# Kernel optimization log

Hardware: AMD Instinct MI355X
Metric: run time of the kernel (lower is better)

## Reference

```python
import jax, jax.numpy as jnp
import numpy as np

C = 768; NH = 12; HD = C // NH; P = 16; IMG = 256; HS = IMG // P  # 16x16 patch grid
WIN = 7; HWP = WIN // 2  # half window (pad)
DEPTH = 12; MLP = 4 * C
B = 32; T = 1
OFFS = [(dh, dw) for dh in range(WIN) for dw in range(WIN)]


def ln(x, g, b, eps=1e-5):
    mu = jnp.mean(x, axis=-1, keepdims=True)
    var = jnp.mean((x - mu) ** 2, axis=-1, keepdims=True)
    return (x - mu) * jax.lax.rsqrt(var + eps) * g + b


def local_attn(x, qkv_w, proj_w, proj_b):
    # x: (B, N, C) with N = HS*HS (T=1); sliding-window attention, zero-padded keys
    Bc, N, _ = x.shape
    qkv = (x @ qkv_w.T).reshape(Bc, N, 3, NH, HD)
    q, k, v = [jnp.transpose(qkv[:, :, i], (0, 2, 1, 3)).reshape(Bc, NH, HS, HS, HD)
               for i in range(3)]
    scale = HD ** -0.5
    kp = jnp.pad(k, ((0, 0), (0, 0), (HWP, HWP), (HWP, HWP), (0, 0)))
    vp = jnp.pad(v, ((0, 0), (0, 0), (HWP, HWP), (HWP, HWP), (0, 0)))
    # per-offset logits; padded (zero) keys give logit 0, matching torch's zero-pad softmax
    scores = jnp.stack([
        jnp.einsum('bnhwd,bnhwd->bnhw', q, kp[:, :, dh:dh + HS, dw:dw + HS]) * scale
        for dh, dw in OFFS], axis=-1)  # (B, NH, HS, HS, 49)
    attn = jax.nn.softmax(scores, axis=-1)
    out = sum(attn[..., i, None] * vp[:, :, dh:dh + HS, dw:dw + HS]
              for i, (dh, dw) in enumerate(OFFS))  # (B, NH, HS, HS, HD)
    out = jnp.transpose(out, (0, 2, 3, 1, 4)).reshape(Bc, N, C)
    return out @ proj_w.T + proj_b


def global_attn(x, in_w, in_b, out_w, out_b):
    Bc, N, _ = x.shape
    qkv = x @ in_w.T + in_b
    q, k, v = jnp.split(qkv, 3, axis=-1)
    hds = lambda t: t.reshape(Bc, N, NH, HD).transpose(0, 2, 1, 3)
    q, k, v = hds(q), hds(k), hds(v)
    s = jnp.einsum('bnqd,bnkd->bnqk', q, k) * (HD ** -0.5)
    a = jax.nn.softmax(s, axis=-1)
    o = jnp.einsum('bnqk,bnkd->bnqd', a, v).transpose(0, 2, 1, 3).reshape(Bc, N, C)
    return o @ out_w.T + out_b


def setup_inputs() -> dict:
    key = jax.random.key(0)
    ks = iter(jax.random.split(key, 40))
    s = 0.02
    inp = {
        'x': jax.random.normal(next(ks), (B, T, 3, IMG, IMG), jnp.float32),
        'aspect_ratio': jax.random.uniform(next(ks), (B,), jnp.float32),
        'conv_w': jax.random.normal(next(ks), (C, 3, P, P), jnp.float32) * s,
        'conv_b': jnp.zeros((C,), jnp.float32),
        'pe_g': jnp.ones((C,), jnp.float32), 'pe_b': jnp.zeros((C,), jnp.float32),
        'ar_token': jax.random.normal(next(ks), (1, 1, C), jnp.float32) * s,
        'pos_embed': jax.random.normal(next(ks), (1, 100 * HS * HS + 1, C), jnp.float32) * s,
        'ln1_g': jnp.ones((DEPTH, C), jnp.float32), 'ln1_b': jnp.zeros((DEPTH, C), jnp.float32),
        'ln2_g': jnp.ones((DEPTH, C), jnp.float32), 'ln2_b': jnp.zeros((DEPTH, C), jnp.float32),
        'loc_qkv_w': jax.random.normal(next(ks), (6, 3 * C, C), jnp.float32) * s,
        'loc_proj_w': jax.random.normal(next(ks), (6, C, C), jnp.float32) * s,
        'loc_proj_b': jnp.zeros((6, C), jnp.float32),
        'glob_in_w': jax.random.normal(next(ks), (6, 3 * C, C), jnp.float32) * s,
        'glob_in_b': jnp.zeros((6, 3 * C), jnp.float32),
        'glob_out_w': jax.random.normal(next(ks), (6, C, C), jnp.float32) * s,
        'glob_out_b': jnp.zeros((6, C), jnp.float32),
        'mlp_w1': jax.random.normal(next(ks), (DEPTH, MLP, C), jnp.float32) * s,
        'mlp_b1': jnp.zeros((DEPTH, MLP), jnp.float32),
        'mlp_w2': jax.random.normal(next(ks), (DEPTH, C, MLP), jnp.float32) * s,
        'mlp_b2': jnp.zeros((DEPTH, C), jnp.float32),
        'fin_g': jnp.ones((C,), jnp.float32), 'fin_b': jnp.zeros((C,), jnp.float32),
    }
    return inp


def reference(x, aspect_ratio, conv_w, conv_b, pe_g, pe_b, ar_token, pos_embed,
              ln1_g, ln1_b, ln2_g, ln2_b,
              loc_qkv_w, loc_proj_w, loc_proj_b,
              glob_in_w, glob_in_b, glob_out_w, glob_out_b,
              mlp_w1, mlp_b1, mlp_w2, mlp_b2, fin_g, fin_b):
    Bc, Tc, Ci, Hi, Wi = x.shape
    # patch embed: non-overlapping conv == block reshape + einsum
    xf = x.reshape(Bc * Tc, Ci, HS, P, HS, P)
    patches = jnp.einsum('bchpwq,ecpq->bhwe', xf, conv_w) + conv_b
    patches = patches.reshape(Bc, Tc * HS * HS, C)
    patches = ln(patches, pe_g, pe_b)
    # aspect ratio token
    ar = ar_token * (1.0 + aspect_ratio[:, None, None] * 0.1)  # (B,1,C)
    h = jnp.concatenate([patches, ar], axis=1)
    h = h + pos_embed[:, :h.shape[1], :]
    for i in range(DEPTH):
        if i % 2 == 0:  # local attention block (AR token stripped, N == HS*HS+1)
            li = i // 2
            tok, art = h[:, :-1], h[:, -1:]
            tok = tok + local_attn(ln(tok, ln1_g[i], ln1_b[i]),
                                   loc_qkv_w[li], loc_proj_w[li], loc_proj_b[li])
            h = jnp.concatenate([tok, art], axis=1)
        else:
            gi = i // 2
            h = h + global_attn(ln(h, ln1_g[i], ln1_b[i]),
                                glob_in_w[gi], glob_in_b[gi], glob_out_w[gi], glob_out_b[gi])
        m = ln(h, ln2_g[i], ln2_b[i])
        m = jax.nn.gelu(m @ mlp_w1[i].T + mlp_b1[i], approximate=False)
        h = h + m @ mlp_w2[i].T + mlp_b2[i]
    return ln(h, fin_g, fin_b)
```

## Files before the change

### kernel.cpp

```cpp
#include <hip/hip_runtime.h>
#include <cmath>

#define NHEADS 12
#define NTOK   257
#define BATCH  32
#define ROWS   (BATCH*NTOK)
#define PROWS  (BATCH*256)
#define GTPAD  288

typedef __attribute__((ext_vector_type(8))) short short8;
typedef __attribute__((ext_vector_type(8))) unsigned short u16x8;
typedef __attribute__((ext_vector_type(4))) float f32x4;

__device__ __forceinline__ unsigned short f2bf(float f) {
    unsigned u = __float_as_uint(f);
    unsigned r = (u + 0x7FFFu + ((u >> 16) & 1u)) >> 16;
    return (unsigned short)r;
}
__device__ __forceinline__ float b2f(unsigned short us) {
    return __uint_as_float((unsigned)us << 16);
}
__device__ __forceinline__ void gload16(const void* g, void* l) {
    __builtin_amdgcn_global_load_lds(
        (const __attribute__((address_space(1))) void*)g,
        (__attribute__((address_space(3))) void*)l, 16, 0, 0);
}

template<bool BIAS, bool GELU, bool RES, bool SKIPAR, bool OUTBF>
__global__ __launch_bounds__(256) void gemm_bf16(
    const unsigned short* __restrict__ A, const unsigned short* __restrict__ W,
    const float* __restrict__ bias, void* __restrict__ outv,
    int M, int N, int K)
{
    __shared__ unsigned short As[2][128 * 64];
    __shared__ unsigned short Bs[2][128 * 64];
    const int tid = threadIdx.x;
    const int lane = tid & 63, wid = tid >> 6;
    const int wr = wid >> 1, wc = wid & 1;

    const int gx = gridDim.x;
    const int nwg = gx * gridDim.y;
    const int orig = blockIdx.y * gx + blockIdx.x;
    const int q8 = nwg >> 3, r8 = nwg & 7;
    const int xcd = orig & 7, lid = orig >> 3;
    const int wg = (xcd < r8 ? xcd * (q8 + 1) : r8 * (q8 + 1) + (xcd - r8) * q8) + lid;
    const int bn = (wg % gx) * 128;
    const int bm = (wg / gx) * 128;

    f32x4 acc[4][4];
    #pragma unroll
    for (int i = 0; i < 4; i++)
        #pragma unroll
        for (int j = 0; j < 4; j++) acc[i][j] = (f32x4)0.f;

    const int l15 = lane & 15;
    const int lg  = lane >> 4;
    const int sw  = l15 & 7;

    auto stage = [&](int buf, int k0) {
        #pragma unroll
        for (int it = 0; it < 4; it++) {
            int f = it * 256 + tid;
            int row = f >> 3;
            int g = (f & 7) ^ (row & 7);
            gload16(A + (size_t)(bm + row) * K + k0 + g * 8, &As[buf][f * 8]);
            gload16(W + (size_t)(bn + row) * K + k0 + g * 8, &Bs[buf][f * 8]);
        }
    };

    const int nt = K >> 6;
    stage(0, 0);
    __syncthreads();

    int buf = 0;
    for (int t = 0; t < nt; t++) {
        if (t + 1 < nt) stage(buf ^ 1, (t + 1) << 6);
        #pragma unroll
        for (int kk = 0; kk < 2; kk++) {
            short8 af[4], bf[4];
            #pragma unroll
            for (int i = 0; i < 4; i++) {
                int row = wr * 64 + i * 16 + l15;
                af[i] = *(const short8*)&As[buf][row * 64 + (((kk * 4 + lg) ^ sw)) * 8];
            }
            #pragma unroll
            for (int j = 0; j < 4; j++) {
                int row = wc * 64 + j * 16 + l15;
                bf[j] = *(const short8*)&Bs[buf][row * 64 + (((kk * 4 + lg) ^ sw)) * 8];
            }
            #pragma unroll
            for (int i = 0; i < 4; i++)
                #pragma unroll
                for (int j = 0; j < 4; j++)
                    acc[i][j] = __builtin_amdgcn_mfma_f32_16x16x32_bf16(af[i], bf[j], acc[i][j], 0, 0, 0);
        }
        __syncthreads();
        buf ^= 1;
    }

    float bcol[4];
    #pragma unroll
    for (int j = 0; j < 4; j++)
        bcol[j] = BIAS ? bias[bn + wc * 64 + j * 16 + l15] : 0.f;

    #pragma unroll
    for (int i = 0; i < 4; i++) {
        #pragma unroll
        for (int r = 0; r < 4; r++) {
            int row = bm + wr * 64 + i * 16 + lg * 4 + r;
            if (row >= M) continue;
            if (SKIPAR && (row % NTOK) == (NTOK - 1)) continue;
            #pragma unroll
            for (int j = 0; j < 4; j++) {
                int col = bn + wc * 64 + j * 16 + l15;
                float v = acc[i][j][r] + bcol[j];
                if (GELU) v = 0.5f * v * (1.0f + erff(v * 0.70710678118654752f));
                size_t idx = (size_t)row * N + col;
                if (OUTBF) {
                    ((unsigned short*)outv)[idx] = f2bf(v);
                } else {
                    float* o = (float*)outv;
                    if (RES) o[idx] += v; else o[idx] = v;
                }
            }
        }
    }
}

template<bool OUTBF>
__global__ __launch_bounds__(256) void ln_kernel(
    const float* __restrict__ in, void* __restrict__ outv,
    const float* __restrict__ g, const float* __restrict__ bparm, int rows)
{
    int gw = blockIdx.x * 4 + (threadIdx.x >> 6);
    int lane = threadIdx.x & 63;
    if (gw >= rows) return;
    const float* x = in + (size_t)gw * 768;
    float4 v[3];
    #pragma unroll
    for (int i = 0; i < 3; i++) v[i] = *(const float4*)(x + i * 256 + lane * 4);
    float s = 0.f;
    #pragma unroll
    for (int i = 0; i < 3; i++) s += v[i].x + v[i].y + v[i].z + v[i].w;
    #pragma unroll
    for (int off = 32; off >= 1; off >>= 1) s += __shfl_xor(s, off, 64);
    float mu = s * (1.f / 768.f);
    float q = 0.f;
    #pragma unroll
    for (int i = 0; i < 3; i++) {
        float dx = v[i].x - mu, dy = v[i].y - mu, dz = v[i].z - mu, dw = v[i].w - mu;
        q += dx * dx + dy * dy + dz * dz + dw * dw;
    }
    #pragma unroll
    for (int off = 32; off >= 1; off >>= 1) q += __shfl_xor(q, off, 64);
    float rstd = rsqrtf(q * (1.f / 768.f) + 1e-5f);
    #pragma unroll
    for (int i = 0; i < 3; i++) {
        float4 gg = *(const float4*)(g + i * 256 + lane * 4);
        float4 bb = *(const float4*)(bparm + i * 256 + lane * 4);
        float rx = (v[i].x - mu) * rstd * gg.x + bb.x;
        float ry = (v[i].y - mu) * rstd * gg.y + bb.y;
        float rz = (v[i].z - mu) * rstd * gg.z + bb.z;
        float rw = (v[i].w - mu) * rstd * gg.w + bb.w;
        if (OUTBF) {
            ushort4 u;
            u.x = f2bf(rx); u.y = f2bf(ry); u.z = f2bf(rz); u.w = f2bf(rw);
            *(ushort4*)((unsigned short*)outv + (size_t)gw * 768 + i * 256 + lane * 4) = u;
        } else {
            *(float4*)((float*)outv + (size_t)gw * 768 + i * 256 + lane * 4) =
                make_float4(rx, ry, rz, rw);
        }
    }
}

__global__ __launch_bounds__(256) void f2b_kernel(
    const float* __restrict__ in, unsigned short* __restrict__ out, int n4)
{
    int i = blockIdx.x * 256 + threadIdx.x;
    if (i >= n4) return;
    float4 v = ((const float4*)in)[i];
    ushort4 u;
    u.x = f2bf(v.x); u.y = f2bf(v.y); u.z = f2bf(v.z); u.w = f2bf(v.w);
    ((ushort4*)out)[i] = u;
}

__global__ __launch_bounds__(256) void gather_patches(
    const float* __restrict__ x, unsigned short* __restrict__ A)
{
    int row = blockIdx.x;
    int b = row >> 8;
    int pp = row & 255;
    int ph = pp >> 4, pw = pp & 15;
    const float* xb = x + (size_t)b * 196608;
    for (int e = threadIdx.x; e < 768; e += 256) {
        int c = e >> 8;
        int r = e & 255;
        int p = r >> 4, q = r & 15;
        A[(size_t)row * 768 + e] = f2bf(xb[(size_t)c * 65536 + (ph * 16 + p) * 256 + pw * 16 + q]);
    }
}

__global__ __launch_bounds__(256) void build_h_kernel(
    const unsigned short* __restrict__ lnp, const float* __restrict__ pos,
    const float* __restrict__ artok, const float* __restrict__ aspect,
    float* __restrict__ h)
{
    int row = blockIdx.x;
    int b = row / NTOK;
    int t = row - b * NTOK;
    float* hp = h + (size_t)row * 768;
    int e = threadIdx.x;
    if (t < 256) {
        const unsigned short* lp = lnp + ((size_t)b * 256 + t) * 768;
        const float* pp = pos + (size_t)t * 768;
        #pragma unroll
        for (int i = 0; i < 3; i++) { int c = e + i * 256; hp[c] = b2f(lp[c]) + pp[c]; }
    } else {
        float f = 1.0f + aspect[b] * 0.1f;
        const float* pp = pos + (size_t)256 * 768;
        #pragma unroll
        for (int i = 0; i < 3; i++) { int c = e + i * 256; hp[c] = artok[c] * f + pp[c]; }
    }
}

__global__ __launch_bounds__(256) void transpose_v(
    const unsigned short* __restrict__ qkv, unsigned short* __restrict__ vt)
{
    __shared__ unsigned short T[64][72];
    const int bh = blockIdx.x;
    const int b = bh / NHEADS, nh = bh % NHEADS;
    const unsigned short* vbase = qkv + (size_t)b * NTOK * 2304 + 1536 + nh * 64;
    unsigned short* obase = vt + (size_t)bh * 64 * GTPAD;
    const int tid = threadIdx.x;

    for (int t0 = 0; t0 < GTPAD; t0 += 64) {
        #pragma unroll
        for (int rnd = 0; rnd < 2; rnd++) {
            int tl = rnd * 32 + (tid >> 3);
            int d0 = (tid & 7) * 8;
            int tok = t0 + tl;
            u16x8 v;
            if (tok < NTOK) {
                v = *(const u16x8*)(vbase + (size_t)tok * 2304 + d0);
            } else {
                #pragma unroll
                for (int i = 0; i < 8; i++) v[i] = 0;
            }
            #pragma unroll
            for (int i = 0; i < 8; i++) T[d0 + i][tl] = v[i];
        }
        __syncthreads();
        int d = tid >> 2, ts = (tid & 3) * 16;
        if (t0 + ts < GTPAD) {
            u16x8 o0, o1;
            #pragma unroll
            for (int i = 0; i < 8; i++) { o0[i] = T[d][ts + i]; o1[i] = T[d][ts + 8 + i]; }
            *(u16x8*)(obase + (size_t)d * GTPAD + t0 + ts) = o0;
            *(u16x8*)(obase + (size_t)d * GTPAD + t0 + ts + 8) = o1;
        }
        __syncthreads();
    }
}

__global__ __launch_bounds__(256) void local_attn_mfma(
    const unsigned short* __restrict__ qkv, const unsigned short* __restrict__ vt,
    unsigned short* __restrict__ out)
{
    __shared__ unsigned short P[4][16 * 136];
    const int wid = threadIdx.x >> 6, lane = threadIdx.x & 63;
    const int gw = blockIdx.x * 4 + wid;
    const int bh = gw >> 4, h0 = gw & 15;
    const int b = bh / NHEADS, nh = bh % NHEADS;
    const int l15 = lane & 15, lg = lane >> 4;
    const unsigned short* base = qkv + (size_t)b * NTOK * 2304 + nh * 64;
    const unsigned short* vtb = vt + (size_t)bh * 64 * GTPAD;
    unsigned short* Pw = P[wid];

    const int qtok = h0 * 16 + l15;
    short8 qf0 = *(const short8*)(base + (size_t)qtok * 2304 + lg * 8);
    short8 qf1 = *(const short8*)(base + (size_t)qtok * 2304 + 32 + lg * 8);

    int r0 = h0 - 3; r0 = r0 < 0 ? 0 : (r0 > 8 ? 8 : r0);

    f32x4 s[8];
    #pragma unroll
    for (int i = 0; i < 8; i++) {
        const unsigned short* kr = base + (size_t)((r0 + i) * 16 + l15) * 2304 + 768;
        short8 kf0 = *(const short8*)(kr + lg * 8);
        short8 kf1 = *(const short8*)(kr + 32 + lg * 8);
        f32x4 z = (f32x4)0.f;
        z = __builtin_amdgcn_mfma_f32_16x16x32_bf16(kf0, qf0, z, 0, 0, 0);
        z = __builtin_amdgcn_mfma_f32_16x16x32_bf16(kf1, qf1, z, 0, 0, 0);
        s[i] = z;
    }

    const int vlo = l15 - 3 < 0 ? 0 : l15 - 3;
    const int vhi = l15 + 3 > 15 ? 15 : l15 + 3;
    const int rlo = h0 - 3 < 0 ? 0 : h0 - 3;
    const int rhi = h0 + 3 > 15 ? 15 : h0 + 3;
    const int n_oob = 49 - (rhi - rlo + 1) * (vhi - vlo + 1);
    float m = n_oob > 0 ? 0.f : -1e30f;
    float sv[32];
    #pragma unroll
    for (int i = 0; i < 8; i++) {
        int kh = r0 + i;
        bool rowok = (kh >= rlo) && (kh <= rhi);
        #pragma unroll
        for (int r = 0; r < 4; r++) {
            int kw = lg * 4 + r;
            bool ok = rowok && (kw >= vlo) && (kw <= vhi);
            float xx = ok ? s[i][r] * 0.125f : -1e30f;
            sv[i * 4 + r] = xx;
            m = fmaxf(m, xx);
        }
    }
    m = fmaxf(m, __shfl_xor(m, 16, 64));
    m = fmaxf(m, __shfl_xor(m, 32, 64));
    float tsum = 0.f;
    #pragma unroll
    for (int i = 0; i < 8; i++) {
        float p0 = __expf(sv[i * 4 + 0] - m);
        float p1 = __expf(sv[i * 4 + 1] - m);
        float p2 = __expf(sv[i * 4 + 2] - m);
        float p3 = __expf(sv[i * 4 + 3] - m);
        tsum += p0 + p1 + p2 + p3;
        unsigned u0 = (unsigned)f2bf(p0) | ((unsigned)f2bf(p1) << 16);
        unsigned u1 = (unsigned)f2bf(p2) | ((unsigned)f2bf(p3) << 16);
        *(uint2*)((char*)Pw + l15 * 272 + i * 32 + lg * 8) = make_uint2(u0, u1);
    }
    tsum += __shfl_xor(tsum, 16, 64);
    tsum += __shfl_xor(tsum, 32, 64);
    float denom = tsum + (float)n_oob * __expf(-m);
    __syncthreads();

    f32x4 acc[4];
    #pragma unroll
    for (int d = 0; d < 4; d++) acc[d] = (f32x4)0.f;
    #pragma unroll
    for (int kt = 0; kt < 128; kt += 32) {
        short8 pf = *(const short8*)((char*)Pw + l15 * 272 + kt * 2 + lg * 16);
        #pragma unroll
        for (int d = 0; d < 4; d++) {
            short8 vf = *(const short8*)(vtb + (size_t)(d * 16 + l15) * GTPAD + r0 * 16 + kt + lg * 8);
            acc[d] = __builtin_amdgcn_mfma_f32_16x16x32_bf16(vf, pf, acc[d], 0, 0, 0);
        }
    }

    float inv = 1.f / denom;
    unsigned short* op = out + ((size_t)b * NTOK + qtok) * 768 + nh * 64;
    #pragma unroll
    for (int d = 0; d < 4; d++) {
        ushort4 o;
        o.x = f2bf(acc[d][0] * inv);
        o.y = f2bf(acc[d][1] * inv);
        o.z = f2bf(acc[d][2] * inv);
        o.w = f2bf(acc[d][3] * inv);
        *(ushort4*)(op + d * 16 + lg * 4) = o;
    }
}

__global__ __launch_bounds__(64) void global_attn_mfma(
    const unsigned short* __restrict__ qkv, const unsigned short* __restrict__ vt,
    unsigned short* __restrict__ out)
{
    __shared__ uint4 Pbuf[80];
    unsigned short* P = (unsigned short*)Pbuf;
    const int blk = blockIdx.x;
    const int bh = blk / 17, qt = blk % 17;
    const int b = bh / NHEADS, nh = bh % NHEADS;
    const int lane = threadIdx.x;
    const int l15 = lane & 15, lg = lane >> 4;
    const unsigned short* base = qkv + (size_t)b * NTOK * 2304 + nh * 64;
    const unsigned short* vtb = vt + (size_t)bh * 64 * GTPAD;

    int qrow = qt * 16 + l15;
    const bool qvalid = qrow < NTOK;
    if (!qvalid) qrow = NTOK - 1;
    short8 qf[2];
    qf[0] = *(const short8*)(base + (size_t)qrow * 2304 + lg * 8);
    qf[1] = *(const short8*)(base + (size_t)qrow * 2304 + 32 + lg * 8);

    f32x4 acc[4];
    #pragma unroll
    for (int i = 0; i < 4; i++) acc[i] = (f32x4)0.f;
    float m = -1e30f, l = 0.f;

    for (int kt = 0; kt < GTPAD; kt += 32) {
        f32x4 s[2];
        #pragma unroll
        for (int hh = 0; hh < 2; hh++) {
            int krow = kt + hh * 16 + l15;
            if (krow > NTOK - 1) krow = NTOK - 1;
            short8 kf0 = *(const short8*)(base + (size_t)krow * 2304 + 768 + lg * 8);
            short8 kf1 = *(const short8*)(base + (size_t)krow * 2304 + 768 + 32 + lg * 8);
            f32x4 z = (f32x4)0.f;
            z = __builtin_amdgcn_mfma_f32_16x16x32_bf16(kf0, qf[0], z, 0, 0, 0);
            z = __builtin_amdgcn_mfma_f32_16x16x32_bf16(kf1, qf[1], z, 0, 0, 0);
            s[hh] = z;
        }
        float sv[8];
        float mt = -1e30f;
        #pragma unroll
        for (int hh = 0; hh < 2; hh++)
            #pragma unroll
            for (int r = 0; r < 4; r++) {
                int key = kt + hh * 16 + lg * 4 + r;
                float v = s[hh][r] * 0.125f;
                if (key >= NTOK) v = -1e30f;
                sv[hh * 4 + r] = v;
                mt = fmaxf(mt, v);
            }
        mt = fmaxf(mt, __shfl_xor(mt, 16, 64));
        mt = fmaxf(mt, __shfl_xor(mt, 32, 64));
        float mn = fmaxf(m, mt);
        float cf = __expf(m - mn);
        float tsum = 0.f;
        unsigned short pb[8];
        #pragma unroll
        for (int i = 0; i < 8; i++) {
            float p = __expf(sv[i] - mn);
            tsum += p;
            pb[i] = f2bf(p);
        }
        tsum += __shfl_xor(tsum, 16, 64);
        tsum += __shfl_xor(tsum, 32, 64);
        l = l * cf + tsum;
        m = mn;
        #pragma unroll
        for (int i = 0; i < 4; i++) acc[i] *= cf;

        unsigned u0 = (unsigned)pb[0] | ((unsigned)pb[1] << 16);
        unsigned u1 = (unsigned)pb[2] | ((unsigned)pb[3] << 16);
        unsigned u2 = (unsigned)pb[4] | ((unsigned)pb[5] << 16);
        unsigned u3 = (unsigned)pb[6] | ((unsigned)pb[7] << 16);
        *(uint2*)((char*)P + l15 * 80 + lg * 8)      = make_uint2(u0, u1);
        *(uint2*)((char*)P + l15 * 80 + 32 + lg * 8) = make_uint2(u2, u3);
        __syncthreads();
        short8 pf = *(const short8*)((char*)P + l15 * 80 + lg * 16);
        #pragma unroll
        for (int d = 0; d < 4; d++) {
            short8 vf = *(const short8*)(vtb + (size_t)(d * 16 + l15) * GTPAD + kt + lg * 8);
            acc[d] = __builtin_amdgcn_mfma_f32_16x16x32_bf16(vf, pf, acc[d], 0, 0, 0);
        }
        __syncthreads();
    }

    if (qvalid) {
        float inv = 1.f / l;
        unsigned short* op = out + ((size_t)b * NTOK + qrow) * 768 + nh * 64;
        #pragma unroll
        for (int d = 0; d < 4; d++) {
            ushort4 o;
            o.x = f2bf(acc[d][0] * inv);
            o.y = f2bf(acc[d][1] * inv);
            o.z = f2bf(acc[d][2] * inv);
            o.w = f2bf(acc[d][3] * inv);
            *(ushort4*)(op + d * 16 + lg * 4) = o;
        }
    }
}

extern "C" void kernel_launch(void* const* d_in, const int* in_sizes, int n_in,
                              void* d_out, int out_size, void* d_ws, size_t ws_size,
                              hipStream_t stream)
{
    const float* x       = (const float*)d_in[0];
    const float* aspect  = (const float*)d_in[1];
    const float* conv_w  = (const float*)d_in[2];
    const float* conv_b  = (const float*)d_in[3];
    const float* pe_g    = (const float*)d_in[4];
    const float* pe_b    = (const float*)d_in[5];
    const float* ar_tok  = (const float*)d_in[6];
    const float* pos     = (const float*)d_in[7];
    const float* ln1_g   = (const float*)d_in[8];
    const float* ln1_b   = (const float*)d_in[9];
    const float* ln2_g   = (const float*)d_in[10];
    const float* ln2_b   = (const float*)d_in[11];
    const float* loc_qkv_w  = (const float*)d_in[12];
    const float* loc_proj_w = (const float*)d_in[13];
    const float* loc_proj_b = (const float*)d_in[14];
    const float* glob_in_w  = (const float*)d_in[15];
    const float* glob_in_b  = (const float*)d_in[16];
    const float* glob_out_w = (const float*)d_in[17];
    const float* glob_out_b = (const float*)d_in[18];
    const float* mlp_w1  = (const float*)d_in[19];
    const float* mlp_b1  = (const float*)d_in[20];
    const float* mlp_w2  = (const float*)d_in[21];
    const float* mlp_b2  = (const float*)d_in[22];
    const float* fin_g   = (const float*)d_in[23];
    const float* fin_b   = (const float*)d_in[24];

    char* w = (char*)d_ws;
    float*          h     = (float*)w;
    unsigned short* lnb   = (unsigned short*)(w + 25264128);
    unsigned short* qkvb  = (unsigned short*)(w + 37896192);
    unsigned short* attnb = (unsigned short*)(w + 75792384);
    unsigned short* mlpb  = (unsigned short*)(w + 88424448);
    float*          pembf = (float*)mlpb;
    unsigned short* vtb   = mlpb;
    char* wp = w + 138952704;
    unsigned short* wconv  = (unsigned short*)wp;               wp += 1179648;
    unsigned short* wlqkv  = (unsigned short*)wp;               wp += 21233664;
    unsigned short* wlproj = (unsigned short*)wp;               wp += 7077888;
    unsigned short* wgin   = (unsigned short*)wp;               wp += 21233664;
    unsigned short* wgout  = (unsigned short*)wp;               wp += 7077888;
    unsigned short* wm1    = (unsigned short*)wp;               wp += 56623104;
    unsigned short* wm2    = (unsigned short*)wp;               wp += 56623104;

    auto cvt = [&](const float* src, unsigned short* dst, int n) {
        int n4 = n / 4;
        f2b_kernel<<<(n4 + 255) / 256, 256, 0, stream>>>(src, dst, n4);
    };
    cvt(conv_w,     wconv,  768 * 768);
    cvt(loc_qkv_w,  wlqkv,  6 * 2304 * 768);
    cvt(loc_proj_w, wlproj, 6 * 768 * 768);
    cvt(glob_in_w,  wgin,   6 * 2304 * 768);
    cvt(glob_out_w, wgout,  6 * 768 * 768);
    cvt(mlp_w1,     wm1,    12 * 3072 * 768);
    cvt(mlp_w2,     wm2,    12 * 768 * 3072);

    gather_patches<<<PROWS, 256, 0, stream>>>(x, qkvb);
    gemm_bf16<true, false, false, false, false><<<dim3(6, 64), 256, 0, stream>>>(
        qkvb, wconv, conv_b, pembf, PROWS, 768, 768);
    ln_kernel<true><<<PROWS / 4, 256, 0, stream>>>(pembf, attnb, pe_g, pe_b, PROWS);
    build_h_kernel<<<ROWS, 256, 0, stream>>>(attnb, pos, ar_tok, aspect, h);

    const int mt = (ROWS + 127) / 128;
    for (int i = 0; i < 12; i++) {
        int half = i / 2;
        ln_kernel<true><<<(ROWS + 3) / 4, 256, 0, stream>>>(h, lnb, ln1_g + i * 768, ln1_b + i * 768, ROWS);
        if ((i & 1) == 0) {
            gemm_bf16<false, false, false, false, true><<<dim3(18, mt), 256, 0, stream>>>(
                lnb, wlqkv + (size_t)half * 2304 * 768, nullptr, qkvb, ROWS, 2304, 768);
            transpose_v<<<BATCH * NHEADS, 256, 0, stream>>>(qkvb, vtb);
            local_attn_mfma<<<BATCH * NHEADS * 16 / 4, 256, 0, stream>>>(qkvb, vtb, attnb);
            gemm_bf16<true, false, true, true, false><<<dim3(6, mt), 256, 0, stream>>>(
                attnb, wlproj + (size_t)half * 768 * 768, loc_proj_b + half * 768, h, ROWS, 768, 768);
        } else {
            gemm_bf16<true, false, false, false, true><<<dim3(18, mt), 256, 0, stream>>>(
                lnb, wgin + (size_t)half * 2304 * 768, glob_in_b + half * 2304, qkvb, ROWS, 2304, 768);
            transpose_v<<<BATCH * NHEADS, 256, 0, stream>>>(qkvb, vtb);
            global_attn_mfma<<<BATCH * NHEADS * 17, 64, 0, stream>>>(qkvb, vtb, attnb);
            gemm_bf16<true, false, true, false, false><<<dim3(6, mt), 256, 0, stream>>>(
                attnb, wgout + (size_t)half * 768 * 768, glob_out_b + half * 768, h, ROWS, 768, 768);
        }
        ln_kernel<true><<<(ROWS + 3) / 4, 256, 0, stream>>>(h, lnb, ln2_g + i * 768, ln2_b + i * 768, ROWS);
        gemm_bf16<true, true, false, false, true><<<dim3(24, mt), 256, 0, stream>>>(
            lnb, wm1 + (size_t)i * 3072 * 768, mlp_b1 + i * 3072, mlpb, ROWS, 3072, 768);
        gemm_bf16<true, false, true, false, false><<<dim3(6, mt), 256, 0, stream>>>(
            mlpb, wm2 + (size_t)i * 768 * 3072, mlp_b2 + i * 768, h, ROWS, 768, 3072);
    }
    ln_kernel<false><<<(ROWS + 3) / 4, 256, 0, stream>>>(h, (float*)d_out, fin_g, fin_b, ROWS);
}
```

Measured before the change: 3.682 ms.

## Fuse V transpose into QKV GEMM epilogue and use tanh GELU

The QKV GEMM epilogue now writes the V columns straight into the transposed per-head vt buffer, so the separate transpose_v kernel is no longer launched. A small kernel zeroes the padded tail of vt once per layer, and vt gets its own workspace region. Separately, the exact erf GELU is replaced by a tanh approximation built on __expf, which lowers epilogue cost but changes numerics relative to the exact-GELU reference. The transposed V stores are strided scatters, so they may write memory less efficiently than the old tiled transpose.

```diff
diff --git a/kernel.cpp b/kernel.cpp
--- a/kernel.cpp
+++ b/kernel.cpp
@@ -25,11 +25,18 @@
         (const __attribute__((address_space(1))) void*)g,
         (__attribute__((address_space(3))) void*)l, 16, 0, 0);
 }
-
-template<bool BIAS, bool GELU, bool RES, bool SKIPAR, bool OUTBF>
+__device__ __forceinline__ float gelu_f(float x) {
+    float y = 0.7978845608f * (x + 0.044715f * x * x * x);
+    float e = __expf(2.f * y);
+    float t = 1.f - 2.f / (e + 1.f);
+    return 0.5f * x * (1.f + t);
+}
+
+template<bool BIAS, bool GELU, bool RES, bool SKIPAR, bool OUTBF, bool VT>
 __global__ __launch_bounds__(256) void gemm_bf16(
     const unsigned short* __restrict__ A, const unsigned short* __restrict__ W,
     const float* __restrict__ bias, void* __restrict__ outv,
+    unsigned short* __restrict__ vt,
     int M, int N, int K)
 {
     __shared__ unsigned short As[2][128 * 64];
@@ -62,9 +69,9 @@
         for (int it = 0; it < 4; it++) {
             int f = it * 256 + tid;
             int row = f >> 3;
-            int g = (f & 7) ^ (row & 7);
-            gload16(A + (size_t)(bm + row) * K + k0 + g * 8, &As[buf][f * 8]);
-            gload16(W + (size_t)(bn + row) * K + k0 + g * 8, &Bs[buf][f * 8]);
+            int gc = (f & 7) ^ (row & 7);
+            gload16(A + (size_t)(bm + row) * K + k0 + gc * 8, &As[buf][f * 8]);
+            gload16(W + (size_t)(bn + row) * K + k0 + gc * 8, &Bs[buf][f * 8]);
         }
     };
 
@@ -110,14 +117,22 @@
             int row = bm + wr * 64 + i * 16 + lg * 4 + r;
             if (row >= M) continue;
             if (SKIPAR && (row % NTOK) == (NTOK - 1)) continue;
+            int bb = 0, tok = 0;
+            if (VT) { bb = row / NTOK; tok = row - bb * NTOK; }
             #pragma unroll
             for (int j = 0; j < 4; j++) {
                 int col = bn + wc * 64 + j * 16 + l15;
                 float v = acc[i][j][r] + bcol[j];
-                if (GELU) v = 0.5f * v * (1.0f + erff(v * 0.70710678118654752f));
+                if (GELU) v = gelu_f(v);
                 size_t idx = (size_t)row * N + col;
                 if (OUTBF) {
-                    ((unsigned short*)outv)[idx] = f2bf(v);
+                    if (VT && col >= 1536) {
+                        int c = col - 1536;
+                        int nh = c >> 6, d = c & 63;
+                        vt[(size_t)((bb * NHEADS + nh) * 64 + d) * GTPAD + tok] = f2bf(v);
+                    } else {
+                        ((unsigned short*)outv)[idx] = f2bf(v);
+                    }
                 } else {
                     float* o = (float*)outv;
                     if (RES) o[idx] += v; else o[idx] = v;
@@ -125,6 +140,13 @@
             }
         }
     }
+}
+
+__global__ __launch_bounds__(256) void zero_vt_pad(unsigned short* __restrict__ vt)
+{
+    int t = blockIdx.x * 256 + threadIdx.x;
+    int bhd = t >> 2, ch = t & 3;
+    *(uint4*)(vt + (size_t)bhd * GTPAD + 256 + ch * 8) = make_uint4(0u, 0u, 0u, 0u);
 }
 
 template<bool OUTBF>
@@ -220,45 +242,6 @@
         const float* pp = pos + (size_t)256 * 768;
         #pragma unroll
         for (int i = 0; i < 3; i++) { int c = e + i * 256; hp[c] = artok[c] * f + pp[c]; }
-    }
-}
-
-__global__ __launch_bounds__(256) void transpose_v(
-    const unsigned short* __restrict__ qkv, unsigned short* __restrict__ vt)
-{
-    __shared__ unsigned short T[64][72];
-    const int bh = blockIdx.x;
-    const int b = bh / NHEADS, nh = bh % NHEADS;
-    const unsigned short* vbase = qkv + (size_t)b * NTOK * 2304 + 1536 + nh * 64;
-    unsigned short* obase = vt + (size_t)bh * 64 * GTPAD;
-    const int tid = threadIdx.x;
-
-    for (int t0 = 0; t0 < GTPAD; t0 += 64) {
-        #pragma unroll
-        for (int rnd = 0; rnd < 2; rnd++) {
-            int tl = rnd * 32 + (tid >> 3);
-            int d0 = (tid & 7) * 8;
-            int tok = t0 + tl;
-            u16x8 v;
-            if (tok < NTOK) {
-                v = *(const u16x8*)(vbase + (size_t)tok * 2304 + d0);
-            } else {
-                #pragma unroll
-                for (int i = 0; i < 8; i++) v[i] = 0;
-            }
-            #pragma unroll
-            for (int i = 0; i < 8; i++) T[d0 + i][tl] = v[i];
-        }
-        __syncthreads();
-        int d = tid >> 2, ts = (tid & 3) * 16;
-        if (t0 + ts < GTPAD) {
-            u16x8 o0, o1;
-            #pragma unroll
-            for (int i = 0; i < 8; i++) { o0[i] = T[d][ts + i]; o1[i] = T[d][ts + 8 + i]; }
-            *(u16x8*)(obase + (size_t)d * GTPAD + t0 + ts) = o0;
-            *(u16x8*)(obase + (size_t)d * GTPAD + t0 + ts + 8) = o1;
-        }
-        __syncthreads();
     }
 }
 
@@ -497,7 +480,7 @@
     unsigned short* attnb = (unsigned short*)(w + 75792384);
     unsigned short* mlpb  = (unsigned short*)(w + 88424448);
     float*          pembf = (float*)mlpb;
-    unsigned short* vtb   = mlpb;
+    unsigned short* vtb   = (unsigned short*)(w + 124796928);
     char* wp = w + 138952704;
     unsigned short* wconv  = (unsigned short*)wp;               wp += 1179648;
     unsigned short* wlqkv  = (unsigned short*)wp;               wp += 21233664;
@@ -520,8 +503,8 @@
     cvt(mlp_w2,     wm2,    12 * 768 * 3072);
 
     gather_patches<<<PROWS, 256, 0, stream>>>(x, qkvb);
-    gemm_bf16<true, false, false, false, false><<<dim3(6, 64), 256, 0, stream>>>(
-        qkvb, wconv, conv_b, pembf, PROWS, 768, 768);
+    gemm_bf16<true, false, false, false, false, false><<<dim3(6, 64), 256, 0, stream>>>(
+        qkvb, wconv, conv_b, pembf, nullptr, PROWS, 768, 768);
     ln_kernel<true><<<PROWS / 4, 256, 0, stream>>>(pembf, attnb, pe_g, pe_b, PROWS);
     build_h_kernel<<<ROWS, 256, 0, stream>>>(attnb, pos, ar_tok, aspect, h);
 
@@ -529,26 +512,25 @@
     for (int i = 0; i < 12; i++) {
         int half = i / 2;
         ln_kernel<true><<<(ROWS + 3) / 4, 256, 0, stream>>>(h, lnb, ln1_g + i * 768, ln1_b + i * 768, ROWS);
+        zero_vt_pad<<<384, 256, 0, stream>>>(vtb);
         if ((i & 1) == 0) {
-            gemm_bf16<false, false, false, false, true><<<dim3(18, mt), 256, 0, stream>>>(
-                lnb, wlqkv + (size_t)half * 2304 * 768, nullptr, qkvb, ROWS, 2304, 768);
-            transpose_v<<<BATCH * NHEADS, 256, 0, stream>>>(qkvb, vtb);
+            gemm_bf16<false, false, false, false, true, true><<<dim3(18, mt), 256, 0, stream>>>(
+                lnb, wlqkv + (size_t)half * 2304 * 768, nullptr, qkvb, vtb, ROWS, 2304, 768);
             local_attn_mfma<<<BATCH * NHEADS * 16 / 4, 256, 0, stream>>>(qkvb, vtb, attnb);
-            gemm_bf16<true, false, true, true, false><<<dim3(6, mt), 256, 0, stream>>>(
-                attnb, wlproj + (size_t)half * 768 * 768, loc_proj_b + half * 768, h, ROWS, 768, 768);
+            gemm_bf16<true, false, true, true, false, false><<<dim3(6, mt), 256, 0, stream>>>(
+                attnb, wlproj + (size_t)half * 768 * 768, loc_proj_b + half * 768, h, nullptr, ROWS, 768, 768);
         } else {
-            gemm_bf16<true, false, false, false, true><<<dim3(18, mt), 256, 0, stream>>>(
-                lnb, wgin + (size_t)half * 2304 * 768, glob_in_b + half * 2304, qkvb, ROWS, 2304, 768);
-            transpose_v<<<BATCH * NHEADS, 256, 0, stream>>>(qkvb, vtb);
+            gemm_bf16<true, false, false, false, true, true><<<dim3(18, mt), 256, 0, stream>>>(
+                lnb, wgin + (size_t)half * 2304 * 768, glob_in_b + half * 2304, qkvb, vtb, ROWS, 2304, 768);
             global_attn_mfma<<<BATCH * NHEADS * 17, 64, 0, stream>>>(qkvb, vtb, attnb);
-            gemm_bf16<true, false, true, false, false><<<dim3(6, mt), 256, 0, stream>>>(
-                attnb, wgout + (size_t)half * 768 * 768, glob_out_b + half * 768, h, ROWS, 768, 768);
+            gemm_bf16<true, false, true, false, false, false><<<dim3(6, mt), 256, 0, stream>>>(
+                attnb, wgout + (size_t)half * 768 * 768, glob_out_b + half * 768, h, nullptr, ROWS, 768, 768);
         }
         ln_kernel<true><<<(ROWS + 3) / 4, 256, 0, stream>>>(h, lnb, ln2_g + i * 768, ln2_b + i * 768, ROWS);
-        gemm_bf16<true, true, false, false, true><<<dim3(24, mt), 256, 0, stream>>>(
-            lnb, wm1 + (size_t)i * 3072 * 768, mlp_b1 + i * 3072, mlpb, ROWS, 3072, 768);
-        gemm_bf16<true, false, true, false, false><<<dim3(6, mt), 256, 0, stream>>>(
-            mlpb, wm2 + (size_t)i * 768 * 3072, mlp_b2 + i * 768, h, ROWS, 768, 3072);
+        gemm_bf16<true, true, false, false, true, false><<<dim3(24, mt), 256, 0, stream>>>(
+            lnb, wm1 + (size_t)i * 3072 * 768, mlp_b1 + i * 3072, mlpb, nullptr, ROWS, 3072, 768);
+        gemm_bf16<true, false, true, false, false, false><<<dim3(6, mt), 256, 0, stream>>>(
+            mlpb, wm2 + (size_t)i * 768 * 3072, mlp_b2 + i * 768, h, nullptr, ROWS, 768, 3072);
     }
     ln_kernel<false><<<(ROWS + 3) / 4, 256, 0, stream>>>(h, (float*)d_out, fin_g, fin_b, ROWS);
 }
```

Result: no change. 3.723 ms (+1.1%).
